# Performance work log

Measured on AMD Instinct MI355X. Metric: run time of the kernel, lower is better.

The kernel has to match this reference:

```python
import jax, jax.numpy as jnp
import numpy as np

EPS = 1e-5

def layer_norm(x, gamma, beta):
    mu = jnp.mean(x, axis=-1, keepdims=True)
    var = jnp.mean(jnp.square(x - mu), axis=-1, keepdims=True)
    return (x - mu) * jax.lax.rsqrt(var + EPS) * gamma + beta

def setup_inputs() -> dict:
    key = jax.random.key(0)
    ks = jax.random.split(key, 12)
    B, S, D = 2, 4096, 1024
    H = 4 * D
    s_in = 1.0 / np.sqrt(D)
    s_h = 1.0 / np.sqrt(H)
    return {
        "input_embedding": jax.random.normal(ks[0], (B, S, D), dtype=jnp.float32),
        "Wq": jax.random.uniform(ks[1], (D, D), jnp.float32, -s_in, s_in),
        "bq": jax.random.uniform(ks[2], (D,), jnp.float32, -s_in, s_in),
        "Wk": jax.random.uniform(ks[3], (D, D), jnp.float32, -s_in, s_in),
        "bk": jax.random.uniform(ks[4], (D,), jnp.float32, -s_in, s_in),
        "Wv": jax.random.uniform(ks[5], (D, D), jnp.float32, -s_in, s_in),
        "bv": jax.random.uniform(ks[6], (D,), jnp.float32, -s_in, s_in),
        "W1": jax.random.uniform(ks[7], (D, H), jnp.float32, -s_in, s_in),
        "b1": jax.random.uniform(ks[8], (H,), jnp.float32, -s_in, s_in),
        "W2": jax.random.uniform(ks[9], (H, D), jnp.float32, -s_h, s_h),
        "b2": jax.random.uniform(ks[10], (D,), jnp.float32, -s_h, s_h),
        "gamma": jnp.ones((D,), jnp.float32),
        "beta": jnp.zeros((D,), jnp.float32),
    }

def reference(input_embedding, Wq, bq, Wk, bk, Wv, bv, W1, b1, W2, b2, gamma, beta):
    D = input_embedding.shape[-1]
    # projections
    k = input_embedding @ Wk + bk
    q = input_embedding @ Wq + bq
    v = input_embedding @ Wv + bv
    # NOTE: original calls attention(k, q, v) so Q<-k, K<-q, V<-v (faithful quirk)
    scores = jnp.einsum('bsd,btd->bst', k, q) / jnp.sqrt(jnp.float32(D))
    attn = jax.nn.softmax(scores, axis=-1)
    attn_out = jnp.einsum('bst,btd->bsd', attn, v)  # dropout = identity (eval)
    x = layer_norm(input_embedding + attn_out, gamma, beta)
    # feed-forward (GELU exact, dropout identity)
    h = jax.nn.gelu(x @ W1 + b1, approximate=False)
    ff = h @ W2 + b2
    return layer_norm(x + ff, gamma, beta)
```

## Files before the change

kernel.cpp:

```cpp
#include <hip/hip_runtime.h>
#include <hip/hip_bf16.h>
#include <stdint.h>

#define AS1 __attribute__((address_space(1)))
#define AS3 __attribute__((address_space(3)))

typedef __bf16 bf16x8 __attribute__((ext_vector_type(8)));
typedef __bf16 bf16x4 __attribute__((ext_vector_type(4)));
typedef float  f32x4  __attribute__((ext_vector_type(4)));

__device__ __forceinline__ void gld_lds16(const void* g, void* l) {
    __builtin_amdgcn_global_load_lds((AS1 void*)g, (AS3 void*)l, 16, 0, 0);
}

__global__ __launch_bounds__(256, 2)
void gemm_nt(const __bf16* __restrict__ A, const __bf16* __restrict__ B,
             __bf16* __restrict__ C, const float* __restrict__ bias,
             int K, int lda, int ldb, int ldc,
             long sA, long sB, long sC, long sBias,
             int ep, float scale)
{
    __shared__ __bf16 smA[2][4096];
    __shared__ __bf16 smB[2][4096];
    const int t  = threadIdx.x;
    const int l  = t & 63;
    const int w  = t >> 6;
    const int wm = w >> 1, wn = w & 1;
    const int lr = l & 15;
    const int lq = l >> 4;
    const long bz = blockIdx.z;
    const int br = blockIdx.y, bc = blockIdx.x;

    const int swc = ((t & 3) ^ ((t >> 3) & 3)) * 8;
    const __bf16* ag = A + bz * sA + (size_t)(br * 128 + (t >> 2)) * lda + swc;
    const __bf16* bg = B + bz * sB + (size_t)(bc * 128 + (t >> 2)) * ldb + swc;
    const size_t a64 = (size_t)64 * lda, b64 = (size_t)64 * ldb;

    f32x4 acc[4][4];
    const f32x4 zero4 = {0.f, 0.f, 0.f, 0.f};
#pragma unroll
    for (int i = 0; i < 4; ++i)
#pragma unroll
        for (int j = 0; j < 4; ++j) acc[i][j] = zero4;

    const int paOff = (wm * 64 + lr) * 32 + ((lq ^ ((lr >> 1) & 3)) * 8);
    const int pbOff = (wn * 64 + lr) * 32 + ((lq ^ ((lr >> 1) & 3)) * 8);

    auto prefetch = [&](int b) {
        __bf16* la = &smA[b][t * 8];
        __bf16* lb = &smB[b][t * 8];
        gld_lds16(ag,       la);
        gld_lds16(ag + a64, la + 2048);
        gld_lds16(bg,       lb);
        gld_lds16(bg + b64, lb + 2048);
        ag += 32; bg += 32;
    };
    auto compute = [&](int b) {
        const __bf16* pa = &smA[b][paOff];
        const __bf16* pb = &smB[b][pbOff];
        bf16x8 af[4], bfr[4];
#pragma unroll
        for (int i = 0; i < 4; ++i) af[i]  = *(const bf16x8*)(pa + i * 16 * 32);
#pragma unroll
        for (int j = 0; j < 4; ++j) bfr[j] = *(const bf16x8*)(pb + j * 16 * 32);
#pragma unroll
        for (int i = 0; i < 4; ++i)
#pragma unroll
            for (int j = 0; j < 4; ++j)
                acc[i][j] = __builtin_amdgcn_mfma_f32_16x16x32_bf16(af[i], bfr[j], acc[i][j], 0, 0, 0);
    };

    const int nkt = K >> 5;
    prefetch(0);
    for (int kt = 0; kt < nkt; kt += 2) {
        __syncthreads();
        if (kt + 1 < nkt) prefetch(1);
        compute(0);
        __syncthreads();
        if (kt + 2 < nkt) prefetch(0);
        compute(1);
    }

    const int r0 = br * 128 + wm * 64 + lq * 4;
    const int c0 = bc * 128 + wn * 64 + lr;
    C += bz * sC;
    const float* bs = bias ? bias + bz * sBias : nullptr;
#pragma unroll
    for (int i = 0; i < 4; ++i) {
#pragma unroll
        for (int j = 0; j < 4; ++j) {
            const int col = c0 + j * 16;
            const float bcol = (ep != 1 && bs) ? bs[col] : 0.f;
#pragma unroll
            for (int r = 0; r < 4; ++r) {
                const long row = r0 + i * 16 + r;
                const long idx = row * (long)ldc + col;
                const float v = acc[i][j][r];
                if (ep == 0) {
                    C[idx] = (__bf16)(v + bcol);
                } else if (ep == 1) {
                    C[idx] = (__bf16)(v * scale);
                } else {
                    const float u = v + bcol;
                    C[idx] = (__bf16)(0.5f * u * (1.f + erff(u * 0.70710678118f)));
                }
            }
        }
    }
}

__global__ __launch_bounds__(256)
void conv_bf16(const float* __restrict__ in, __bf16* __restrict__ out)
{
    const long i = (long)blockIdx.x * 256 + threadIdx.x;
    const float4 f = ((const float4*)in)[i];
    bf16x4 o = {(__bf16)f.x, (__bf16)f.y, (__bf16)f.z, (__bf16)f.w};
    ((bf16x4*)out)[i] = o;
}

__global__ void tr_f32_bf16(const float* __restrict__ in, __bf16* __restrict__ out,
                            int K, int N)
{
    __shared__ float tl[32][33];
    const int x = threadIdx.x, y = threadIdx.y;
    const int n0 = blockIdx.x * 32, k0 = blockIdx.y * 32;
#pragma unroll
    for (int i = 0; i < 4; ++i)
        tl[y + 8 * i][x] = in[(size_t)(k0 + y + 8 * i) * N + n0 + x];
    __syncthreads();
#pragma unroll
    for (int i = 0; i < 4; ++i)
        out[(size_t)(n0 + y + 8 * i) * K + k0 + x] = (__bf16)tl[x][y + 8 * i];
}

__global__ void tr_bf16(const __bf16* __restrict__ in, __bf16* __restrict__ out,
                        int R, int C)
{
    in  += (size_t)blockIdx.z * R * C;
    out += (size_t)blockIdx.z * R * C;
    __shared__ __bf16 tl[32][33];
    const int x = threadIdx.x, y = threadIdx.y;
    const int c0 = blockIdx.x * 32, r0 = blockIdx.y * 32;
#pragma unroll
    for (int i = 0; i < 4; ++i)
        tl[y + 8 * i][x] = in[(size_t)(r0 + y + 8 * i) * C + c0 + x];
    __syncthreads();
#pragma unroll
    for (int i = 0; i < 4; ++i)
        out[(size_t)(c0 + y + 8 * i) * R + r0 + x] = tl[x][y + 8 * i];
}

__global__ __launch_bounds__(256)
void softmax_rows(__bf16* __restrict__ S)
{
    __bf16* rp = S + (size_t)blockIdx.x * 4096;
    const int t = threadIdx.x;
    float v[16];
#pragma unroll
    for (int c = 0; c < 2; ++c) {
        const bf16x8 f = ((const bf16x8*)rp)[t + c * 256];
#pragma unroll
        for (int k = 0; k < 8; ++k) v[c * 8 + k] = (float)f[k];
    }
    float mx = v[0];
#pragma unroll
    for (int i = 1; i < 16; ++i) mx = fmaxf(mx, v[i]);
#pragma unroll
    for (int o = 32; o; o >>= 1) mx = fmaxf(mx, __shfl_down(mx, o, 64));
    __shared__ float rm[4], rs[4];
    if ((t & 63) == 0) rm[t >> 6] = mx;
    __syncthreads();
    mx = fmaxf(fmaxf(rm[0], rm[1]), fmaxf(rm[2], rm[3]));
    float s = 0.f;
#pragma unroll
    for (int i = 0; i < 16; ++i) { v[i] = __expf(v[i] - mx); s += v[i]; }
#pragma unroll
    for (int o = 32; o; o >>= 1) s += __shfl_down(s, o, 64);
    if ((t & 63) == 0) rs[t >> 6] = s;
    __syncthreads();
    s = rs[0] + rs[1] + rs[2] + rs[3];
    const float inv = 1.f / s;
#pragma unroll
    for (int c = 0; c < 2; ++c) {
        bf16x8 o8;
#pragma unroll
        for (int k = 0; k < 8; ++k) o8[k] = (__bf16)(v[c * 8 + k] * inv);
        ((bf16x8*)rp)[t + c * 256] = o8;
    }
}

__global__ __launch_bounds__(256)
void ln_residual(const float* __restrict__ af, const __bf16* __restrict__ ab,
                 const __bf16* __restrict__ bb,
                 const float* __restrict__ gamma, const float* __restrict__ beta,
                 float* __restrict__ outf, __bf16* __restrict__ outb)
{
    const long row = blockIdx.x;
    const int t = threadIdx.x;
    float x0, x1, x2, x3;
    if (af) {
        const float4 va = ((const float4*)(af + row * 1024))[t];
        x0 = va.x; x1 = va.y; x2 = va.z; x3 = va.w;
    } else {
        const bf16x4 va = ((const bf16x4*)(ab + row * 1024))[t];
        x0 = (float)va[0]; x1 = (float)va[1]; x2 = (float)va[2]; x3 = (float)va[3];
    }
    {
        const bf16x4 vb = ((const bf16x4*)(bb + row * 1024))[t];
        x0 += (float)vb[0]; x1 += (float)vb[1]; x2 += (float)vb[2]; x3 += (float)vb[3];
    }
    float s = x0 + x1 + x2 + x3;
    float q = x0 * x0 + x1 * x1 + x2 * x2 + x3 * x3;
#pragma unroll
    for (int o = 32; o; o >>= 1) { s += __shfl_down(s, o, 64); q += __shfl_down(q, o, 64); }
    __shared__ float rs[4], rq[4];
    if ((t & 63) == 0) { rs[t >> 6] = s; rq[t >> 6] = q; }
    __syncthreads();
    s = rs[0] + rs[1] + rs[2] + rs[3];
    q = rq[0] + rq[1] + rq[2] + rq[3];
    const float mu  = s * (1.f / 1024.f);
    const float inv = rsqrtf(q * (1.f / 1024.f) - mu * mu + 1e-5f);
    const float4 g  = ((const float4*)gamma)[t];
    const float4 be = ((const float4*)beta)[t];
    const float y0 = (x0 - mu) * inv * g.x + be.x;
    const float y1 = (x1 - mu) * inv * g.y + be.y;
    const float y2 = (x2 - mu) * inv * g.z + be.z;
    const float y3 = (x3 - mu) * inv * g.w + be.w;
    if (outf) ((float4*)(outf + row * 1024))[t] = make_float4(y0, y1, y2, y3);
    if (outb) {
        bf16x4 o4 = {(__bf16)y0, (__bf16)y1, (__bf16)y2, (__bf16)y3};
        ((bf16x4*)outb)[row * 256 + t] = o4;
    }
}

__global__ __launch_bounds__(256)
void fill_diag(float* __restrict__ out, float v, long n)
{
    const long i = (long)blockIdx.x * 256 + threadIdx.x;
    if (i < n) out[i] = v;
}

extern "C" void kernel_launch(void* const* d_in, const int* in_sizes, int n_in,
                              void* d_out, int out_size, void* d_ws, size_t ws_size,
                              hipStream_t stream)
{
    const float* X  = (const float*)d_in[0];
    const float* Wq = (const float*)d_in[1];
    const float* bq = (const float*)d_in[2];
    const float* Wk = (const float*)d_in[3];
    const float* bk = (const float*)d_in[4];
    const float* Wv = (const float*)d_in[5];
    const float* bv = (const float*)d_in[6];
    const float* W1 = (const float*)d_in[7];
    const float* b1 = (const float*)d_in[8];
    const float* W2 = (const float*)d_in[9];
    const float* b2 = (const float*)d_in[10];
    const float* gamma = (const float*)d_in[11];
    const float* beta  = (const float*)d_in[12];
    float* out = (float*)d_out;

    const int S = 4096, D = 1024, H = 4096;
    const int M = 2 * S;

    const size_t szW  = 8388608;
    const size_t szP  = 16777216;
    const size_t oW1T = 0;
    const size_t oW2T = szW;
    const size_t oQP  = 2 * szW;
    const size_t oKP  = oQP + szP;
    const size_t oVP  = oKP + szP;
    const size_t oVT  = oVP + szP;
    const size_t oAO  = oVT + szP;
    const size_t oSL  = oAO + szP;
    const size_t need1 = oSL + 33554432;
    const size_t need2 = oSL + szP;

    int Rs;
    if (ws_size >= need1)      Rs = 4096;
    else if (ws_size >= need2) Rs = 2048;
    else {
        fill_diag<<<dim3((out_size + 255) / 256), dim3(256), 0, stream>>>(
            out, (float)(ws_size >> 20), out_size);
        return;
    }

    char* ws = (char*)d_ws;
    __bf16* W1T = (__bf16*)(ws + oW1T);
    __bf16* W2T = (__bf16*)(ws + oW2T);
    __bf16* QP  = (__bf16*)(ws + oQP);
    __bf16* FF  = (__bf16*)(ws + oQP);
    __bf16* KP  = (__bf16*)(ws + oKP);
    __bf16* HB  = (__bf16*)(ws + oKP);
    __bf16* VP  = (__bf16*)(ws + oVP);
    __bf16* VT  = (__bf16*)(ws + oVT);
    __bf16* WQT = (__bf16*)(ws + oAO);
    float*  BIAS= (float*)(ws + oAO + 6291456);
    __bf16* AO  = (__bf16*)(ws + oAO);
    __bf16* XB  = (__bf16*)(ws + oSL);
    __bf16* SL  = (__bf16*)(ws + oSL);
    __bf16* XLNB= (__bf16*)(ws + oSL);

    const dim3 t256(256);
    const dim3 t32x8(32, 8);

    conv_bf16<<<dim3(M * D / 1024), t256, 0, stream>>>(X, XB);
    tr_f32_bf16<<<dim3(D / 32, D / 32), t32x8, 0, stream>>>(Wq, WQT, D, D);
    tr_f32_bf16<<<dim3(D / 32, D / 32), t32x8, 0, stream>>>(Wk, WQT + (size_t)D * D, D, D);
    tr_f32_bf16<<<dim3(D / 32, D / 32), t32x8, 0, stream>>>(Wv, WQT + (size_t)2 * D * D, D, D);
    tr_f32_bf16<<<dim3(H / 32, D / 32), t32x8, 0, stream>>>(W1, W1T, D, H);
    tr_f32_bf16<<<dim3(D / 32, H / 32), t32x8, 0, stream>>>(W2, W2T, H, D);
    hipMemcpyAsync(BIAS,         bq, D * 4, hipMemcpyDeviceToDevice, stream);
    hipMemcpyAsync(BIAS + D,     bk, D * 4, hipMemcpyDeviceToDevice, stream);
    hipMemcpyAsync(BIAS + 2 * D, bv, D * 4, hipMemcpyDeviceToDevice, stream);

    gemm_nt<<<dim3(D / 128, M / 128, 3), t256, 0, stream>>>(
        XB, WQT, QP, BIAS, D, D, D, D,
        0, (long)D * D, (long)M * D, D, 0, 0.f);

    tr_bf16<<<dim3(D / 32, S / 32, 2), t32x8, 0, stream>>>(VP, VT, S, D);

    for (int b = 0; b < 2; ++b) {
        for (int c = 0; c < S / Rs; ++c) {
            const __bf16* Ak = KP + (size_t)(b * S + c * Rs) * D;
            gemm_nt<<<dim3(S / 128, Rs / 128), t256, 0, stream>>>(
                Ak, QP + (size_t)b * S * D, SL, nullptr, D, D, D, S,
                0, 0, 0, 0, 1, 0.03125f);
            softmax_rows<<<dim3(Rs), t256, 0, stream>>>(SL);
            gemm_nt<<<dim3(D / 128, Rs / 128), t256, 0, stream>>>(
                SL, VT + (size_t)b * D * S, AO + (size_t)(b * S + c * Rs) * D, nullptr,
                S, S, S, D, 0, 0, 0, 0, 0, 0.f);
        }
    }

    ln_residual<<<dim3(M), t256, 0, stream>>>(X, nullptr, AO, gamma, beta, nullptr, XLNB);

    gemm_nt<<<dim3(H / 128, M / 128), t256, 0, stream>>>(
        XLNB, W1T, HB, b1, D, D, D, H, 0, 0, 0, 0, 3, 0.f);

    gemm_nt<<<dim3(D / 128, M / 128), t256, 0, stream>>>(
        HB, W2T, FF, b2, H, H, H, D, 0, 0, 0, 0, 0, 0.f);

    ln_residual<<<dim3(M), t256, 0, stream>>>(nullptr, XLNB, FF, gamma, beta, out, nullptr);
}
```

Before: 723.5 us.

## Split-K the PV and FFN2 GEMMs, tanh-GELU via exp, raise occupancy bound

The attention PV GEMM and the second FFN GEMM are split along K into two halves, each writing a separate bf16 partial buffer. The partials (and the b2 bias) are summed inside the LayerNorm residual kernel, which doubles the grid for these skinny D=1024-column GEMMs. The exact erf GELU is replaced by the tanh-approximation written as a sigmoid with __expf. launch_bounds min-blocks goes from 2 to 4 to raise occupancy. Risks are bf16 rounding of the partial sums, extra memory traffic for the second partial buffer, register spilling under the tighter bound, and a small accuracy change from the GELU approximation.

```diff
diff --git a/kernel.cpp b/kernel.cpp
--- a/kernel.cpp
+++ b/kernel.cpp
@@ -13,7 +13,7 @@
     __builtin_amdgcn_global_load_lds((AS1 void*)g, (AS3 void*)l, 16, 0, 0);
 }
 
-__global__ __launch_bounds__(256, 2)
+__global__ __launch_bounds__(256, 4)
 void gemm_nt(const __bf16* __restrict__ A, const __bf16* __restrict__ B,
              __bf16* __restrict__ C, const float* __restrict__ bias,
              int K, int lda, int ldb, int ldc,
@@ -102,7 +102,8 @@
                     C[idx] = (__bf16)(v * scale);
                 } else {
                     const float u = v + bcol;
-                    C[idx] = (__bf16)(0.5f * u * (1.f + erff(u * 0.70710678118f)));
+                    const float z = 1.59576912f * (u + 0.044715f * u * u * u);
+                    C[idx] = (__bf16)(u / (1.f + __expf(-z)));
                 }
             }
         }
@@ -191,7 +192,8 @@
 
 __global__ __launch_bounds__(256)
 void ln_residual(const float* __restrict__ af, const __bf16* __restrict__ ab,
-                 const __bf16* __restrict__ bb,
+                 const __bf16* __restrict__ bb, const __bf16* __restrict__ bb2,
+                 const float* __restrict__ lnb,
                  const float* __restrict__ gamma, const float* __restrict__ beta,
                  float* __restrict__ outf, __bf16* __restrict__ outb)
 {
@@ -208,6 +210,14 @@
     {
         const bf16x4 vb = ((const bf16x4*)(bb + row * 1024))[t];
         x0 += (float)vb[0]; x1 += (float)vb[1]; x2 += (float)vb[2]; x3 += (float)vb[3];
+    }
+    if (bb2) {
+        const bf16x4 vb = ((const bf16x4*)(bb2 + row * 1024))[t];
+        x0 += (float)vb[0]; x1 += (float)vb[1]; x2 += (float)vb[2]; x3 += (float)vb[3];
+    }
+    if (lnb) {
+        const float4 vb = ((const float4*)lnb)[t];
+        x0 += vb.x; x1 += vb.y; x2 += vb.z; x3 += vb.w;
     }
     float s = x0 + x1 + x2 + x3;
     float q = x0 * x0 + x1 * x1 + x2 * x2 + x3 * x3;
@@ -292,6 +302,7 @@
     __bf16* KP  = (__bf16*)(ws + oKP);
     __bf16* HB  = (__bf16*)(ws + oKP);
     __bf16* VP  = (__bf16*)(ws + oVP);
+    __bf16* AO2 = (__bf16*)(ws + oVP);
     __bf16* VT  = (__bf16*)(ws + oVT);
     __bf16* WQT = (__bf16*)(ws + oAO);
     float*  BIAS= (float*)(ws + oAO + 6291456);
@@ -299,6 +310,7 @@
     __bf16* XB  = (__bf16*)(ws + oSL);
     __bf16* SL  = (__bf16*)(ws + oSL);
     __bf16* XLNB= (__bf16*)(ws + oSL);
+    __bf16* FF2 = (__bf16*)(ws + oSL + szP);
 
     const dim3 t256(256);
     const dim3 t32x8(32, 8);
@@ -319,6 +331,7 @@
 
     tr_bf16<<<dim3(D / 32, S / 32, 2), t32x8, 0, stream>>>(VP, VT, S, D);
 
+    const long sCpv = (long)(AO2 - AO);
     for (int b = 0; b < 2; ++b) {
         for (int c = 0; c < S / Rs; ++c) {
             const __bf16* Ak = KP + (size_t)(b * S + c * Rs) * D;
@@ -326,19 +339,28 @@
                 Ak, QP + (size_t)b * S * D, SL, nullptr, D, D, D, S,
                 0, 0, 0, 0, 1, 0.03125f);
             softmax_rows<<<dim3(Rs), t256, 0, stream>>>(SL);
-            gemm_nt<<<dim3(D / 128, Rs / 128), t256, 0, stream>>>(
+            gemm_nt<<<dim3(D / 128, Rs / 128, 2), t256, 0, stream>>>(
                 SL, VT + (size_t)b * D * S, AO + (size_t)(b * S + c * Rs) * D, nullptr,
-                S, S, S, D, 0, 0, 0, 0, 0, 0.f);
+                S / 2, S, S, D, S / 2, S / 2, sCpv, 0, 0, 0.f);
         }
     }
 
-    ln_residual<<<dim3(M), t256, 0, stream>>>(X, nullptr, AO, gamma, beta, nullptr, XLNB);
+    ln_residual<<<dim3(M), t256, 0, stream>>>(
+        X, nullptr, AO, AO2, nullptr, gamma, beta, nullptr, XLNB);
 
     gemm_nt<<<dim3(H / 128, M / 128), t256, 0, stream>>>(
         XLNB, W1T, HB, b1, D, D, D, H, 0, 0, 0, 0, 3, 0.f);
 
-    gemm_nt<<<dim3(D / 128, M / 128), t256, 0, stream>>>(
-        HB, W2T, FF, b2, H, H, H, D, 0, 0, 0, 0, 0, 0.f);
-
-    ln_residual<<<dim3(M), t256, 0, stream>>>(nullptr, XLNB, FF, gamma, beta, out, nullptr);
-}
+    if (Rs == 4096) {
+        gemm_nt<<<dim3(D / 128, M / 128, 2), t256, 0, stream>>>(
+            HB, W2T, FF, nullptr, H / 2, H, H, D,
+            H / 2, H / 2, (long)(FF2 - FF), 0, 1, 1.0f);
+        ln_residual<<<dim3(M), t256, 0, stream>>>(
+            nullptr, XLNB, FF, FF2, b2, gamma, beta, out, nullptr);
+    } else {
+        gemm_nt<<<dim3(D / 128, M / 128), t256, 0, stream>>>(
+            HB, W2T, FF, b2, H, H, H, D, 0, 0, 0, 0, 0, 0.f);
+        ln_residual<<<dim3(M), t256, 0, stream>>>(
+            nullptr, XLNB, FF, nullptr, nullptr, gamma, beta, out, nullptr);
+    }
+}
```

Result: faster. 698.3 us (-3.5%).
